# Kernel optimization log

Hardware: AMD Instinct MI355X
Metric: run time of the kernel (lower is better)

The kernel has to match this reference:

```python
import jax, jax.numpy as jnp
import numpy as np

NUM_HEAD = 16
D_MODEL = 1024


def setup_inputs() -> dict:
    key = jax.random.key(0)
    k1, k2, k3 = jax.random.split(key, 3)
    B, S = 4, 2048
    x = jax.random.normal(k1, (B, S, D_MODEL), dtype=jnp.float32)
    W_qkv = jax.random.normal(k2, (D_MODEL, 3 * D_MODEL), dtype=jnp.float32) * (D_MODEL ** -0.5)
    b_qkv = jnp.zeros((3 * D_MODEL,), dtype=jnp.float32)
    W_o = jax.random.normal(k3, (D_MODEL, D_MODEL), dtype=jnp.float32) * (D_MODEL ** -0.5)
    b_o = jnp.zeros((D_MODEL,), dtype=jnp.float32)
    return {"x": x, "W_qkv": W_qkv, "b_qkv": b_qkv, "W_o": W_o, "b_o": b_o}


def reference(x, W_qkv, b_qkv, W_o, b_o):
    B, S, dm = x.shape
    H = NUM_HEAD
    hd = dm // H
    qkv = x @ W_qkv + b_qkv                       # [B,S,3*dm]
    qkv = qkv.reshape(B, S, H, 3 * hd).transpose(0, 2, 1, 3)  # [B,H,S,3*hd]
    q, k, v = jnp.split(qkv, 3, axis=-1)          # each [B,H,S,hd]
    scale = jnp.sqrt(jnp.asarray(hd, dtype=q.dtype))
    att = jnp.einsum('bhqd,bhkd->bhqk', q, k) / scale  # [B,H,S,S]
    causal = jnp.tril(jnp.ones((S, S), dtype=bool))    # band_part(ones,-1,0)
    att = jnp.where(causal, att, -jnp.inf)             # additive 0 / -inf mask
    att = jax.nn.softmax(att, axis=-1)
    vals = jnp.einsum('bhqk,bhkd->bhqd', att, v)       # [B,H,S,hd]
    # Faithful to original: reshape WITHOUT transposing heads back (axis scramble)
    vals = vals.reshape(B, S, H * hd)
    return vals @ W_o + b_o
```

## Files before the change

kernel.cpp:

```cpp
#include <hip/hip_runtime.h>
#include <hip/hip_bf16.h>
#include <stdint.h>


typedef __attribute__((ext_vector_type(8))) __bf16 bf16x8;
typedef __attribute__((ext_vector_type(4))) float f32x4;
typedef __attribute__((ext_vector_type(16))) float f32x16;

#define AS_G __attribute__((address_space(1)))
#define AS_L __attribute__((address_space(3)))

__device__ __forceinline__ void gload_lds16(const void* g, void* s) {
  __builtin_amdgcn_global_load_lds((const AS_G void*)g, (AS_L void*)s, 16, 0, 0);
}

__device__ __forceinline__ unsigned cvt_pk_bf16(float lo, float hi) {
  unsigned r;
  asm("v_cvt_pk_bf16_f32 %0, %1, %2" : "=v"(r) : "v"(lo), "v"(hi));
  return r;
}

__device__ __forceinline__ void cvt_T_body(const float* __restrict__ in,
                                           __bf16* __restrict__ out,
                                           int K, int N, int bx, int by,
                                           float (*tile)[33]) {
  int tx = threadIdx.x & 31, ty = threadIdx.x >> 5;
#pragma unroll
  for (int i = 0; i < 32; i += 8)
    tile[ty + i][tx] = in[(size_t)(by * 32 + ty + i) * N + bx * 32 + tx];
  __syncthreads();
#pragma unroll
  for (int i = 0; i < 32; i += 8)
    out[(size_t)(bx * 32 + ty + i) * K + by * 32 + tx] = (__bf16)tile[tx][ty + i];
}

__global__ void fused_cvt_kernel(const float* __restrict__ x,
                                 __bf16* __restrict__ xb,
                                 const float* __restrict__ Wqkv,
                                 __bf16* __restrict__ Wqt,
                                 const float* __restrict__ Wo,
                                 __bf16* __restrict__ Wot) {
  __shared__ float tile[32][33];
  const int bid = blockIdx.x;
  if (bid < 4096) {
    const int i = bid * 256 + threadIdx.x;
    float4 a = ((const float4*)x)[i * 2];
    float4 b = ((const float4*)x)[i * 2 + 1];
    union { __bf16 h[8]; int4 v; } u;
    u.h[0] = (__bf16)a.x; u.h[1] = (__bf16)a.y; u.h[2] = (__bf16)a.z; u.h[3] = (__bf16)a.w;
    u.h[4] = (__bf16)b.x; u.h[5] = (__bf16)b.y; u.h[6] = (__bf16)b.z; u.h[7] = (__bf16)b.w;
    ((int4*)xb)[i] = u.v;
  } else if (bid < 7168) {
    const int t = bid - 4096;
    cvt_T_body(Wqkv, Wqt, 1024, 3072, t % 96, t / 96, tile);
  } else {
    const int t = bid - 7168;
    cvt_T_body(Wo, Wot, 1024, 1024, t % 32, t / 32, tile);
  }
}

template <int MODE>
__global__ __launch_bounds__(512, 4) void gemm256(
    const __bf16* __restrict__ A, const __bf16* __restrict__ Bt,
    const float* __restrict__ bias,
    __bf16* __restrict__ Qb, __bf16* __restrict__ Kb, __bf16* __restrict__ Vtb,
    float* __restrict__ Out) {
  __shared__ char lds[73728];
  const int tid = threadIdx.x;
  const int wv = tid >> 6, lane = tid & 63;
  const int lhi = lane >> 4, llo = lane & 15;
  const int wm = wv >> 1, wn = wv & 1;

  const int wg = blockIdx.x;
  const int xcd = wg & 7, local = wg >> 3;
  const int m0 = (xcd * 4 + (local & 3)) * 256;
  const int n0 = (local >> 2) * 128;

  int SA[2], SB;
#pragma unroll
  for (int j = 0; j < 2; ++j) {
    const int idx = j * 512 + tid;
    const int v = idx >> 3, wl = idx & 7;
    const int wg_ = wl ^ (v & 7);
    SA[j] = ((v << 1) | (wg_ >> 2)) * 1024 + (wg_ & 3) * 8;
  }
  {
    const int v = tid >> 3, wl = tid & 7;
    const int wg_ = wl ^ (v & 7);
    SB = ((v << 1) | (wg_ >> 2)) * 1024 + (wg_ & 3) * 8;
  }
  const __bf16* Asrc = A + (size_t)m0 * 1024;
  const __bf16* Bsrc = Bt + (size_t)n0 * 1024;
  const int wvb = wv * 1024;

#define STAGE_R(b, kc)                                                      \
  gload_lds16(Asrc + SA[0] + (kc) * 32, &lds[(b) * 16384 + wvb]);           \
  gload_lds16(Asrc + SA[1] + (kc) * 32, &lds[(b) * 16384 + 8192 + wvb]);    \
  gload_lds16(Bsrc + SB + (kc) * 32,    &lds[49152 + (b) * 8192 + wvb]);

  f32x4 acc[4][4];
#pragma unroll
  for (int mi = 0; mi < 4; ++mi)
#pragma unroll
    for (int nj = 0; nj < 4; ++nj) acc[mi][nj] = (f32x4){0.f, 0.f, 0.f, 0.f};

  auto aoff = [&](int b, int f) {
    const int r = wm * 64 + f * 16 + llo;
    const int v = r >> 1;
    const int w = ((r & 1) << 2) | lhi;
    return b * 16384 + v * 128 + ((w ^ (v & 7)) << 4);
  };
  auto boff = [&](int b, int f2) {
    const int r = wn * 64 + f2 * 16 + llo;
    const int v = r >> 1;
    const int w = ((r & 1) << 2) | lhi;
    return 49152 + b * 8192 + v * 128 + ((w ^ (v & 7)) << 4);
  };

  auto PH = [&](int c, int sb, int kc) {
    __builtin_amdgcn_s_barrier();
    __builtin_amdgcn_sched_barrier(0);
    bf16x8 fa[4], fb[4];
#pragma unroll
    for (int f = 0; f < 4; ++f) fa[f] = *(const bf16x8*)&lds[aoff(c, f)];
#pragma unroll
    for (int f2 = 0; f2 < 4; ++f2) fb[f2] = *(const bf16x8*)&lds[boff(c, f2)];
    STAGE_R(sb, kc);
    __builtin_amdgcn_sched_barrier(0);
    asm volatile("s_waitcnt lgkmcnt(0)" ::: "memory");
    __builtin_amdgcn_sched_barrier(0);
    __builtin_amdgcn_s_setprio(1);
#pragma unroll
    for (int mi = 0; mi < 4; ++mi)
#pragma unroll
      for (int nj = 0; nj < 4; ++nj)
        acc[mi][nj] = __builtin_amdgcn_mfma_f32_16x16x32_bf16(fa[mi], fb[nj],
                                                              acc[mi][nj], 0, 0, 0);
    __builtin_amdgcn_s_setprio(0);
    __builtin_amdgcn_sched_barrier(0);
    asm volatile("s_waitcnt vmcnt(3)" ::: "memory");
  };

  STAGE_R(0, 0);
  STAGE_R(1, 1);
  __builtin_amdgcn_sched_barrier(0);
  asm volatile("s_waitcnt vmcnt(3)" ::: "memory");

  {
    int c = 0, sb = 2;
    for (int p = 0; p < 32; ++p) {
      const int kc = (p + 2) & 31;
      PH(c, sb, kc);
      if (++c == 3) c = 0;
      if (++sb == 3) sb = 0;
    }
  }
#undef STAGE_R

#pragma unroll
  for (int nj = 0; nj < 4; ++nj) {
    const int col = n0 + wn * 64 + nj * 16 + llo;
    const float bv = bias[col];
    if (MODE == 0) {
      const int h = col / 192, rem = col % 192;
#pragma unroll
      for (int mi = 0; mi < 4; ++mi) {
        const int row0 = m0 + wm * 64 + mi * 16 + lhi * 4;
        const int b = row0 >> 11;
        const int s0 = row0 & 2047;
        const int bh = b * 16 + h;
        f32x4 v = acc[mi][nj];
        if (rem < 64) {
#pragma unroll
          for (int r = 0; r < 4; ++r)
            Qb[((size_t)bh * 2048 + s0 + r) * 64 + rem] =
                (__bf16)((v[r] + bv) * 0.18033688011112042f);
        } else if (rem < 128) {
#pragma unroll
          for (int r = 0; r < 4; ++r)
            Kb[((size_t)bh * 2048 + s0 + r) * 64 + (rem - 64)] = (__bf16)(v[r] + bv);
        } else {
          union { __bf16 h4[4]; int2 v2; } uq;
#pragma unroll
          for (int r = 0; r < 4; ++r) uq.h4[r] = (__bf16)(v[r] + bv);
          *(int2*)&Vtb[((size_t)bh * 64 + (rem - 128)) * 2048 + s0] = uq.v2;
        }
      }
    } else {
#pragma unroll
      for (int mi = 0; mi < 4; ++mi) {
        const int row0 = m0 + wm * 64 + mi * 16 + lhi * 4;
        f32x4 v = acc[mi][nj];
#pragma unroll
        for (int r = 0; r < 4; ++r)
          Out[(size_t)(row0 + r) * 1024 + col] = v[r] + bv;
      }
    }
  }
}


__device__ __forceinline__ void attn_tile(
    const __bf16* __restrict__ ksb, const __bf16* __restrict__ vsb,
    const bf16x8* qf, const f32x16& zz, int kv0, int q0w, int lq, int hi,
    f32x16& o0, f32x16& o1, float& l) {
  const int r0 = lq, r1 = 32 + lq;
  const int fx = (lq & 7) ^ ((lq >> 3) << 1);
  f32x16 s0, s1;
  __builtin_amdgcn_s_setprio(1);
  {
    const int bb = (hi ^ fx) * 8;
    bf16x8 k0 = *(const bf16x8*)&ksb[r0 * 64 + bb];
    bf16x8 k1 = *(const bf16x8*)&ksb[r1 * 64 + bb];
    s0 = __builtin_amdgcn_mfma_f32_32x32x16_bf16(k0, qf[0], zz, 0, 0, 0);
    s1 = __builtin_amdgcn_mfma_f32_32x32x16_bf16(k1, qf[0], zz, 0, 0, 0);
  }
#pragma unroll
  for (int ds = 1; ds < 4; ++ds) {
    const int bb = ((ds * 2 + hi) ^ fx) * 8;
    bf16x8 k0 = *(const bf16x8*)&ksb[r0 * 64 + bb];
    bf16x8 k1 = *(const bf16x8*)&ksb[r1 * 64 + bb];
    s0 = __builtin_amdgcn_mfma_f32_32x32x16_bf16(k0, qf[ds], s0, 0, 0, 0);
    s1 = __builtin_amdgcn_mfma_f32_32x32x16_bf16(k1, qf[ds], s1, 0, 0, 0);
  }
  __builtin_amdgcn_s_setprio(0);

  const int qg = q0w + lq;
  if (kv0 + 63 > q0w) {
#pragma unroll
    for (int reg = 0; reg < 16; ++reg) {
      const int kvl = (reg & 3) + 8 * (reg >> 2) + 4 * hi;
      if (kv0 + kvl > qg) s0[reg] = -1e30f;
      if (kv0 + 32 + kvl > qg) s1[reg] = -1e30f;
    }
  }
#pragma unroll
  for (int i = 0; i < 16; ++i) s0[i] = __builtin_amdgcn_exp2f(s0[i]);
#pragma unroll
  for (int i = 0; i < 16; ++i) s1[i] = __builtin_amdgcn_exp2f(s1[i]);
  float y[8];
#pragma unroll
  for (int i = 0; i < 8; ++i) y[i] = (s0[i] + s0[i + 8]) + (s1[i] + s1[i + 8]);
#pragma unroll
  for (int st = 4; st; st >>= 1)
#pragma unroll
    for (int i = 0; i < st; ++i) y[i] += y[i + st];
  l += y[0] + __shfl_xor(y[0], 32);

#pragma unroll
  for (int ks = 0; ks < 4; ++ks) {
    unsigned pa, pb, pc, pd;
    if (ks < 2) {
      pa = cvt_pk_bf16(s0[ks * 8 + 0], s0[ks * 8 + 1]);
      pb = cvt_pk_bf16(s0[ks * 8 + 2], s0[ks * 8 + 3]);
      pc = cvt_pk_bf16(s0[ks * 8 + 4], s0[ks * 8 + 5]);
      pd = cvt_pk_bf16(s0[ks * 8 + 6], s0[ks * 8 + 7]);
    } else {
      pa = cvt_pk_bf16(s1[(ks - 2) * 8 + 0], s1[(ks - 2) * 8 + 1]);
      pb = cvt_pk_bf16(s1[(ks - 2) * 8 + 2], s1[(ks - 2) * 8 + 3]);
      pc = cvt_pk_bf16(s1[(ks - 2) * 8 + 4], s1[(ks - 2) * 8 + 5]);
      pd = cvt_pk_bf16(s1[(ks - 2) * 8 + 6], s1[(ks - 2) * 8 + 7]);
    }
    asm volatile("v_permlane32_swap_b32 %0, %1" : "+v"(pa), "+v"(pc));
    asm volatile("v_permlane32_swap_b32 %0, %1" : "+v"(pb), "+v"(pd));
    union { unsigned u[4]; bf16x8 v; } pf;
    pf.u[0] = pa; pf.u[1] = pb; pf.u[2] = pc; pf.u[3] = pd;
    const int vb = ((ks * 2 + hi) ^ fx) * 8;
    bf16x8 v0 = *(const bf16x8*)&vsb[r0 * 64 + vb];
    bf16x8 v1 = *(const bf16x8*)&vsb[r1 * 64 + vb];
    o0 = __builtin_amdgcn_mfma_f32_32x32x16_bf16(v0, pf.v, o0, 0, 0, 0);
    o1 = __builtin_amdgcn_mfma_f32_32x32x16_bf16(v1, pf.v, o1, 0, 0, 0);
  }
}

__device__ __forceinline__ void attn_epilogue(
    __bf16* __restrict__ vals, int bh, int q0w, int lq, int hi,
    const f32x16& o0, const f32x16& o1, float l) {
  const float inv = 1.f / l;
  unsigned* outp = (unsigned*)(vals + ((size_t)bh * 2048 + q0w + lq) * 64);
#pragma unroll
  for (int n = 0; n < 2; ++n) {
#pragma unroll
    for (int g = 0; g < 2; ++g) {
      const float e0 = (n ? o1[g * 8 + 0] : o0[g * 8 + 0]) * inv;
      const float e1 = (n ? o1[g * 8 + 1] : o0[g * 8 + 1]) * inv;
      const float e2 = (n ? o1[g * 8 + 2] : o0[g * 8 + 2]) * inv;
      const float e3 = (n ? o1[g * 8 + 3] : o0[g * 8 + 3]) * inv;
      const float e4 = (n ? o1[g * 8 + 4] : o0[g * 8 + 4]) * inv;
      const float e5 = (n ? o1[g * 8 + 5] : o0[g * 8 + 5]) * inv;
      const float e6 = (n ? o1[g * 8 + 6] : o0[g * 8 + 6]) * inv;
      const float e7 = (n ? o1[g * 8 + 7] : o0[g * 8 + 7]) * inv;
      unsigned a = cvt_pk_bf16(e0, e1);
      unsigned a2 = cvt_pk_bf16(e2, e3);
      unsigned b = cvt_pk_bf16(e4, e5);
      unsigned b2 = cvt_pk_bf16(e6, e7);
      asm volatile("v_permlane32_swap_b32 %0, %1" : "+v"(a), "+v"(b));
      asm volatile("v_permlane32_swap_b32 %0, %1" : "+v"(a2), "+v"(b2));
      int4 st = {(int)a, (int)a2, (int)b, (int)b2};
      *(int4*)&outp[(n * 32 + g * 16 + hi * 8) >> 1] = st;
    }
  }
}

__global__ __launch_bounds__(256) void attn_kernel(
    const __bf16* __restrict__ Q, const __bf16* __restrict__ K,
    const __bf16* __restrict__ Vt, __bf16* __restrict__ vals) {
  __shared__ __bf16 Ks[2][4096];
  __shared__ __bf16 Vs[2][4096];
  const int tid = threadIdx.x;
  const int wave = tid >> 6, lane = tid & 63;
  const int lq = lane & 31, hi = lane >> 5;

  const int wg = blockIdx.x + (blockIdx.y << 3);
  const int wgid = (wg & 7) * 128 + (wg >> 3);
  const int local = wgid & 127;
  const int bh = (wgid >> 7) * 8 + (local & 7);
  const int qc = 15 - (local >> 3);
  const int q0w = qc * 128 + wave * 32;
  const int nt = 2 * qc + 2;

  bf16x8 qf[4];
  {
    const __bf16* qp = Q + ((size_t)bh * 2048 + q0w + lq) * 64 + hi * 8;
#pragma unroll
    for (int ds = 0; ds < 4; ++ds) qf[ds] = *(const bf16x8*)(qp + ds * 16);
  }

  f32x16 o0, o1, zz;
#pragma unroll
  for (int i = 0; i < 16; ++i) { o0[i] = 0.f; o1[i] = 0.f; zz[i] = 0.f; }
  float l = 0.f;

  const int sr = tid >> 3, sb_ = tid & 7;
  const int sc = (sb_ ^ ((sr & 7) ^ ((sr >> 3) << 1))) * 8;
  const __bf16* Kg0 = K + ((size_t)bh * 2048 + sr) * 64 + sc;
  const __bf16* Kg1 = Kg0 + 32 * 64;
  const __bf16* Vg0 = Vt + ((size_t)bh * 64 + sr) * 2048 + sc;
  const __bf16* Vg1 = Vg0 + 32 * 2048;
  __bf16* KsW = &Ks[0][0] + wave * 512;
  __bf16* VsW = &Vs[0][0] + wave * 512;

#define STAGE(buf, t)                                                   \
  gload_lds16(Kg0 + (size_t)(t) * 4096, KsW + (buf) * 4096);            \
  gload_lds16(Kg1 + (size_t)(t) * 4096, KsW + (buf) * 4096 + 2048);     \
  gload_lds16(Vg0 + (t) * 64, VsW + (buf) * 4096);                      \
  gload_lds16(Vg1 + (t) * 64, VsW + (buf) * 4096 + 2048);

  STAGE(0, 0);
  __syncthreads();

  for (int t = 0; t < nt; ++t) {
    const int cur = t & 1;
    if (t + 1 < nt) { STAGE(cur ^ 1, t + 1); }
    attn_tile(&Ks[cur][0], &Vs[cur][0], qf, zz, t * 64, q0w, lq, hi, o0, o1, l);
    __syncthreads();
  }
#undef STAGE

  attn_epilogue(vals, bh, q0w, lq, hi, o0, o1, l);
}

extern "C" void kernel_launch(void* const* d_in, const int* in_sizes, int n_in,
                              void* d_out, int out_size, void* d_ws, size_t ws_size,
                              hipStream_t stream) {
  const float* x = (const float*)d_in[0];
  const float* Wqkv = (const float*)d_in[1];
  const float* bqkv = (const float*)d_in[2];
  const float* Wo = (const float*)d_in[3];
  const float* bo = (const float*)d_in[4];
  float* out = (float*)d_out;
  char* ws = (char*)d_ws;

  __bf16* xb  = (__bf16*)(ws);
  __bf16* Wqt = (__bf16*)(ws + 16777216);
  __bf16* Wot = (__bf16*)(ws + 23068672);
  __bf16* Qb  = (__bf16*)(ws + 25165824);
  __bf16* Kb  = (__bf16*)(ws + 41943040);
  __bf16* Vtb = (__bf16*)(ws + 58720256);
  __bf16* vals = xb;

  fused_cvt_kernel<<<8192, 256, 0, stream>>>(x, xb, Wqkv, Wqt, Wo, Wot);
  gemm256<0><<<768, 512, 0, stream>>>(xb, Wqt, bqkv, Qb, Kb, Vtb, nullptr);
  attn_kernel<<<dim3(8, 128), 256, 0, stream>>>(Qb, Kb, Vtb, vals);
  gemm256<1><<<256, 512, 0, stream>>>(vals, Wot, bo, nullptr, nullptr, nullptr, out);
}
```

Before: 152.4 us.

## Compute softmax row sums via MFMA with ones and unroll GEMM phase loop

The per-tile softmax denominator is now accumulated by an extra MFMA that multiplies a ones vector by the bf16 probabilities, replacing the VALU adds and cross-lane shuffle reduction. Separately, the GEMM main loop is restructured into groups of three phases with constant buffer indices so the rotating buffer counters become compile-time constants. The MFMA sum uses the bf16-rounded probabilities, which keeps it consistent with the PV product but adds matrix-core work and another 16-register accumulator.

```diff
diff --git a/kernel.cpp b/kernel.cpp
--- a/kernel.cpp
+++ b/kernel.cpp
@@ -146,15 +146,15 @@
   __builtin_amdgcn_sched_barrier(0);
   asm volatile("s_waitcnt vmcnt(3)" ::: "memory");
 
-  {
-    int c = 0, sb = 2;
-    for (int p = 0; p < 32; ++p) {
-      const int kc = (p + 2) & 31;
-      PH(c, sb, kc);
-      if (++c == 3) c = 0;
-      if (++sb == 3) sb = 0;
-    }
-  }
+#pragma unroll 1
+  for (int p3 = 0; p3 < 10; ++p3) {
+    const int p = p3 * 3;
+    PH(0, 2, (p + 2) & 31);
+    PH(1, 0, (p + 3) & 31);
+    PH(2, 1, (p + 4) & 31);
+  }
+  PH(0, 2, 0);
+  PH(1, 0, 1);
 #undef STAGE_R
 
 #pragma unroll
@@ -202,8 +202,9 @@
 
 __device__ __forceinline__ void attn_tile(
     const __bf16* __restrict__ ksb, const __bf16* __restrict__ vsb,
-    const bf16x8* qf, const f32x16& zz, int kv0, int q0w, int lq, int hi,
-    f32x16& o0, f32x16& o1, float& l) {
+    const bf16x8* qf, const f32x16& zz, const bf16x8& ones,
+    int kv0, int q0w, int lq, int hi,
+    f32x16& o0, f32x16& o1, f32x16& accl) {
   const int r0 = lq, r1 = 32 + lq;
   const int fx = (lq & 7) ^ ((lq >> 3) << 1);
   f32x16 s0, s1;
@@ -238,14 +239,6 @@
   for (int i = 0; i < 16; ++i) s0[i] = __builtin_amdgcn_exp2f(s0[i]);
 #pragma unroll
   for (int i = 0; i < 16; ++i) s1[i] = __builtin_amdgcn_exp2f(s1[i]);
-  float y[8];
-#pragma unroll
-  for (int i = 0; i < 8; ++i) y[i] = (s0[i] + s0[i + 8]) + (s1[i] + s1[i + 8]);
-#pragma unroll
-  for (int st = 4; st; st >>= 1)
-#pragma unroll
-    for (int i = 0; i < st; ++i) y[i] += y[i + st];
-  l += y[0] + __shfl_xor(y[0], 32);
 
 #pragma unroll
   for (int ks = 0; ks < 4; ++ks) {
@@ -270,6 +263,7 @@
     bf16x8 v1 = *(const bf16x8*)&vsb[r1 * 64 + vb];
     o0 = __builtin_amdgcn_mfma_f32_32x32x16_bf16(v0, pf.v, o0, 0, 0, 0);
     o1 = __builtin_amdgcn_mfma_f32_32x32x16_bf16(v1, pf.v, o1, 0, 0, 0);
+    accl = __builtin_amdgcn_mfma_f32_32x32x16_bf16(ones, pf.v, accl, 0, 0, 0);
   }
 }
 
@@ -326,10 +320,12 @@
     for (int ds = 0; ds < 4; ++ds) qf[ds] = *(const bf16x8*)(qp + ds * 16);
   }
 
-  f32x16 o0, o1, zz;
-#pragma unroll
-  for (int i = 0; i < 16; ++i) { o0[i] = 0.f; o1[i] = 0.f; zz[i] = 0.f; }
-  float l = 0.f;
+  f32x16 o0, o1, zz, accl;
+#pragma unroll
+  for (int i = 0; i < 16; ++i) { o0[i] = 0.f; o1[i] = 0.f; zz[i] = 0.f; accl[i] = 0.f; }
+  bf16x8 ones;
+#pragma unroll
+  for (int i = 0; i < 8; ++i) ones[i] = (__bf16)1.0f;
 
   const int sr = tid >> 3, sb_ = tid & 7;
   const int sc = (sb_ ^ ((sr & 7) ^ ((sr >> 3) << 1))) * 8;
@@ -352,12 +348,13 @@
   for (int t = 0; t < nt; ++t) {
     const int cur = t & 1;
     if (t + 1 < nt) { STAGE(cur ^ 1, t + 1); }
-    attn_tile(&Ks[cur][0], &Vs[cur][0], qf, zz, t * 64, q0w, lq, hi, o0, o1, l);
+    attn_tile(&Ks[cur][0], &Vs[cur][0], qf, zz, ones, t * 64, q0w, lq, hi,
+              o0, o1, accl);
     __syncthreads();
   }
 #undef STAGE
 
-  attn_epilogue(vals, bh, q0w, lq, hi, o0, o1, l);
+  attn_epilogue(vals, bh, q0w, lq, hi, o0, o1, accl[0]);
 }
 
 extern "C" void kernel_launch(void* const* d_in, const int* in_sizes, int n_in,
```

Result: no change. 153.8 us (+0.9%).
